# Kernel optimization log

Hardware: AMD Instinct MI355X
Metric: run time of the kernel (lower is better)

## Reference

```python
import jax, jax.numpy as jnp
import numpy as np

B, T, D_IN, D_EMB, D_OUT = 8, 2048, 1024, 1024, 1024


def setup_inputs() -> dict:
    key = jax.random.key(0)
    ks = jax.random.split(key, 7)
    s_in = 1.0 / np.sqrt(D_IN)
    s_emb = 1.0 / np.sqrt(D_EMB)
    return {
        "x": jax.random.normal(ks[0], (B, T, D_IN), dtype=jnp.float32),
        "bias": jax.random.normal(ks[1], (T, T), dtype=jnp.float32) * 0.02,
        "W_qkv": jax.random.uniform(ks[2], (3 * D_EMB, D_IN), jnp.float32, -s_in, s_in),
        "b_qkv": jax.random.uniform(ks[3], (3 * D_EMB,), jnp.float32, -s_in, s_in),
        "W_out": jax.random.uniform(ks[4], (D_OUT, D_EMB), jnp.float32, -s_emb, s_emb),
        "b_out": jax.random.uniform(ks[5], (D_OUT,), jnp.float32, -s_emb, s_emb),
    }


def reference(x, bias, W_qkv, b_qkv, W_out, b_out):
    # fused QKV projection: [B,T,3E]
    qkv = jnp.einsum("bti,ei->bte", x, W_qkv) + b_qkv
    q, k, v = jnp.split(qkv, 3, axis=-1)  # each [B,T,E]
    d_z = q.shape[-1]
    # scaled dot-product logits with additive relative-position bias
    attn = jnp.einsum("btd,bsd->bts", q, k) / jnp.sqrt(jnp.asarray(d_z, q.dtype))
    attn = attn + bias  # [T,T] broadcast over batch
    attn = jax.nn.softmax(attn, axis=-1)
    values = jnp.einsum("bts,bsd->btd", attn, v)  # [B,T,E]
    out = jnp.einsum("bte,oe->bto", values, W_out) + b_out  # [B,T,O]
    return out
```

## Files before the change

### kernel.cpp

```cpp
#include <hip/hip_runtime.h>
#include <hip/hip_bf16.h>

#define B_DIM 8
#define T_DIM 2048
#define E_DIM 1024

typedef __attribute__((ext_vector_type(8))) short short8;
typedef __attribute__((ext_vector_type(4))) float f32x4;
typedef __attribute__((ext_vector_type(4))) int int4v;

__device__ __forceinline__ unsigned short f2bf(float f) {
  union { float f; unsigned u; } v; v.f = f;
  unsigned r = v.u + 0x7fffu + ((v.u >> 16) & 1u);
  return (unsigned short)(r >> 16);
}
__device__ __forceinline__ float bf2f(unsigned short u) {
  union { unsigned u; float f; } v; v.u = ((unsigned)u) << 16;
  return v.f;
}
__device__ __forceinline__ signed char q8(float f, float scale) {
  int q = __float2int_rn(f * scale);
  q = q > 127 ? 127 : (q < -127 ? -127 : q);
  return (signed char)q;
}

__device__ __forceinline__ void async16(const void* g, void* l) {
  __builtin_amdgcn_global_load_lds(
      (const __attribute__((address_space(1))) unsigned int*)g,
      (__attribute__((address_space(3))) unsigned int*)l, 16, 0, 0);
}

__device__ __forceinline__ void storeC(float* p, float v) { *p = v; }
__device__ __forceinline__ void storeC(unsigned short* p, float v) { *p = f2bf(v); }
__device__ __forceinline__ void storeC(signed char* p, float v) { *p = (signed char)(int)v; }

#define QX 31.75f
#define QY 1814.2857f
#define QP 15.875f
#define KDQ_LOGIT 1.7359973e-5f
#define KDQ_PV    0.031496063f

__global__ __launch_bounds__(256) void cvt_bf16(const float4* __restrict__ in,
                                                ushort4* __restrict__ out) {
  size_t i = (size_t)blockIdx.x * 256 + threadIdx.x;
  float4 v = in[i];
  ushort4 o;
  o.x = f2bf(v.x); o.y = f2bf(v.y); o.z = f2bf(v.z); o.w = f2bf(v.w);
  out[i] = o;
}

__global__ __launch_bounds__(256) void cvt_x_dual(const float* __restrict__ x,
                                                  unsigned short* __restrict__ Xb,
                                                  signed char* __restrict__ Xb8,
                                                  signed char* __restrict__ XT8) {
  __shared__ signed char tc[64][65];
  const int t0 = blockIdx.x * 64, i0 = blockIdx.y * 64;
  const int tx = threadIdx.x & 63, ty = threadIdx.x >> 6;
#pragma unroll
  for (int it = 0; it < 16; ++it) {
    int r = it * 4 + ty;
    float f = x[(size_t)(t0 + r) * 1024 + i0 + tx];
    Xb[(size_t)(t0 + r) * 1024 + i0 + tx] = f2bf(f);
    signed char c = q8(f, QX);
    Xb8[(size_t)(t0 + r) * 1024 + i0 + tx] = c;
    tc[r][tx] = c;
  }
  __syncthreads();
#pragma unroll
  for (int it = 0; it < 16; ++it) {
    int r = it * 4 + ty;
    XT8[(size_t)(i0 + r) * 16384 + t0 + tx] = tc[tx][r];
  }
}

__global__ __launch_bounds__(256) void cvt_t64x3(const float* __restrict__ in,
                                                 unsigned short* __restrict__ o0,
                                                 unsigned short* __restrict__ o1,
                                                 unsigned short* __restrict__ o2) {
  __shared__ unsigned short tl[64][65];
  unsigned short* outT = blockIdx.z == 0 ? o0 : (blockIdx.z == 1 ? o1 : o2);
  const float* src = in + (size_t)blockIdx.z * 1024 * 1024;
  const int r0 = blockIdx.x * 64, c0 = blockIdx.y * 64;
  const int tx = threadIdx.x & 63, ty = threadIdx.x >> 6;
#pragma unroll
  for (int it = 0; it < 16; ++it) {
    int r = it * 4 + ty;
    tl[r][tx] = f2bf(src[(size_t)(r0 + r) * 1024 + c0 + tx]);
  }
  __syncthreads();
#pragma unroll
  for (int it = 0; it < 16; ++it) {
    int r = it * 4 + ty;
    outT[(size_t)(c0 + r) * 1024 + r0 + tx] = tl[tx][r];
  }
}

__global__ __launch_bounds__(256) void dotrows2(const unsigned short* __restrict__ W0,
                                                const float* __restrict__ v0,
                                                const float* __restrict__ add0,
                                                float* __restrict__ out0,
                                                const unsigned short* __restrict__ W1,
                                                const float* __restrict__ v1,
                                                float* __restrict__ out1) {
  const int z = blockIdx.y;
  const unsigned short* W = z ? W1 : W0;
  const float* vec = z ? v1 : v0;
  const float scale = z ? 0.03125f : 1.0f;
  const int o = blockIdx.x * 4 + (threadIdx.x >> 6);
  const int lane = threadIdx.x & 63;
  const short8 w0 = *(const short8*)&W[(size_t)o * 1024 + lane * 16];
  const short8 w1 = *(const short8*)&W[(size_t)o * 1024 + lane * 16 + 8];
  float s = 0.f;
#pragma unroll
  for (int j = 0; j < 8; ++j) s += bf2f((unsigned short)w0[j]) * vec[lane * 16 + j];
#pragma unroll
  for (int j = 0; j < 8; ++j) s += bf2f((unsigned short)w1[j]) * vec[lane * 16 + 8 + j];
#pragma unroll
  for (int off = 1; off < 64; off <<= 1) s += __shfl_xor(s, off);
  if (lane == 0) {
    if (z) out1[o] = s * scale;
    else   out0[o] = s + add0[o];
  }
}

__global__ __launch_bounds__(256) void wvec_k(const unsigned short* __restrict__ Xb,
                                              const float* __restrict__ a2,
                                              float* __restrict__ w) {
  const int row = blockIdx.x * 4 + (threadIdx.x >> 6);
  const int lane = threadIdx.x & 63;
  const short8 x0 = *(const short8*)&Xb[(size_t)row * 1024 + lane * 16];
  const short8 x1 = *(const short8*)&Xb[(size_t)row * 1024 + lane * 16 + 8];
  float s = 0.f;
#pragma unroll
  for (int j = 0; j < 8; ++j) s += bf2f((unsigned short)x0[j]) * a2[lane * 16 + j];
#pragma unroll
  for (int j = 0; j < 8; ++j) s += bf2f((unsigned short)x1[j]) * a2[lane * 16 + 8 + j];
#pragma unroll
  for (int off = 1; off < 64; off <<= 1) s += __shfl_xor(s, off);
  if (lane == 0) w[row] = s;
}

__global__ __launch_bounds__(256) void finish_rowsum(const float* __restrict__ psum,
                                                     float* __restrict__ R) {
  const int z = blockIdx.y;
  const int row = blockIdx.x * 256 + threadIdx.x;
  const float* p = psum + (size_t)z * 32 * 2048 + row;
  float s = 0.f;
#pragma unroll
  for (int k = 0; k < 32; ++k) s += p[k * 2048];
  R[(size_t)z * 2048 + row] = s;
}

__global__ __launch_bounds__(256) void gemm128sk(
    const unsigned short* __restrict__ A0, const unsigned short* __restrict__ B0,
    const unsigned short* __restrict__ A1, const unsigned short* __restrict__ B1,
    float* __restrict__ pw) {
  __shared__ __align__(16) unsigned short Al[128 * 32];
  __shared__ __align__(16) unsigned short Bl[128 * 32];
  const int prob = blockIdx.z & 1, slice = blockIdx.z >> 1;
  const unsigned short* A = prob ? A1 : A0;
  const unsigned short* Bmat = prob ? B1 : B0;
  float* C = pw + ((size_t)prob * 4 + slice) * 1048576;
  const int kbase = slice * 256;

  const int tid = threadIdx.x;
  const int wid = tid >> 6, lane = tid & 63;
  const int wm = wid >> 1, wn = wid & 1;
  const int tm = blockIdx.x * 128, tn = blockIdx.y * 128;
  const int l16 = lane & 15, lk = lane >> 4;

  f32x4 acc[4][4];
#pragma unroll
  for (int i = 0; i < 4; ++i)
#pragma unroll
    for (int j = 0; j < 4; ++j) acc[i][j] = (f32x4){0.f, 0.f, 0.f, 0.f};

  const int ks = (lk ^ ((l16 >> 1) & 3)) * 8;

  for (int k0 = kbase; k0 < kbase + 256; k0 += 32) {
    __syncthreads();
#pragma unroll
    for (int it = 0; it < 2; ++it) {
      int chunk = it * 256 + tid;
      int row = chunk >> 2;
      int q = chunk & 3;
      int qs = q ^ ((row >> 1) & 3);
      const char* g = (const char*)(A + (size_t)(tm + row) * 1024 + k0) + qs * 16;
      async16(g, ((char*)Al) + it * 4096 + wid * 1024);
    }
#pragma unroll
    for (int it = 0; it < 2; ++it) {
      int chunk = it * 256 + tid;
      int row = chunk >> 2;
      int q = chunk & 3;
      int qs = q ^ ((row >> 1) & 3);
      const char* g = (const char*)(Bmat + (size_t)(tn + row) * 1024 + k0) + qs * 16;
      async16(g, ((char*)Bl) + it * 4096 + wid * 1024);
    }
    __syncthreads();

    short8 a[4], b[4];
#pragma unroll
    for (int i = 0; i < 4; ++i)
      a[i] = *(const short8*)&Al[(wm * 64 + i * 16 + l16) * 32 + ks];
#pragma unroll
    for (int j = 0; j < 4; ++j)
      b[j] = *(const short8*)&Bl[(wn * 64 + j * 16 + l16) * 32 + ks];
#pragma unroll
    for (int i = 0; i < 4; ++i)
#pragma unroll
      for (int j = 0; j < 4; ++j)
        acc[i][j] = __builtin_amdgcn_mfma_f32_16x16x32_bf16(a[i], b[j], acc[i][j], 0, 0, 0);
  }

#pragma unroll
  for (int i = 0; i < 4; ++i)
#pragma unroll
    for (int j = 0; j < 4; ++j) {
      int col = tn + wn * 64 + j * 16 + l16;
      int rbase = tm + wm * 64 + i * 16 + lk * 4;
#pragma unroll
      for (int r = 0; r < 4; ++r)
        C[(size_t)(rbase + r) * 1024 + col] = acc[i][j][r];
    }
}

__global__ __launch_bounds__(256) void finish_w(const float* __restrict__ pw,
                                                unsigned short* __restrict__ BH,
                                                unsigned short* __restrict__ Wf) {
  const int prob = blockIdx.y;
  const size_t i = ((size_t)blockIdx.x * 256 + threadIdx.x) * 2;
  const float* p = pw + (size_t)prob * 4194304;
  float s0 = 0.f, s1 = 0.f;
#pragma unroll
  for (int k = 0; k < 4; ++k) {
    const float2 v = *(const float2*)(p + (size_t)k * 1048576 + i);
    s0 += v.x; s1 += v.y;
  }
  const float sc = prob ? 1.0f : 0.03125f;
  unsigned short* dst = prob ? Wf : BH;
  dst[i] = f2bf(s0 * sc);
  dst[i + 1] = f2bf(s1 * sc);
}

template <int EPI, typename OutT>
__global__ __launch_bounds__(512, 2) void gemm8p(
    const unsigned short* __restrict__ A, int lda, long long strA,
    const unsigned short* __restrict__ Bm, int ldb, long long strB,
    OutT* __restrict__ C, int ldc, long long strC, int K,
    const float* __restrict__ biasv, float scale) {
  __shared__ __align__(16) char lds[131072];
  const int tid = threadIdx.x;
  const int wid = tid >> 6, lane = tid & 63;
  const int wm = wid >> 2, wn = wid & 3;
  const int l16 = lane & 15, lk = lane >> 4;
  const int zz = blockIdx.z;

  const int nx = gridDim.x;
  const int nwg = nx * gridDim.y;
  const int bid = blockIdx.y * nx + blockIdx.x;
  const int swz = (bid & 7) * (nwg >> 3) + (bid >> 3);
  const int tm = (swz % nx) * 256, tn = (swz / nx) * 256;

  A += (size_t)zz * strA;
  Bm += (size_t)zz * strB;
  C += (size_t)zz * strC;

  const int nt = K >> 6;

  const int q0 = ((lk ^ (l16 & 7)) << 4);
  const int q1 = (((lk | 4) ^ (l16 & 7)) << 4);
  const int srow = lane >> 3;
  const int scol = ((lane & 7) ^ srow) << 3;

  f32x4 acc[8][4];
#pragma unroll
  for (int i = 0; i < 8; ++i)
#pragma unroll
    for (int j = 0; j < 4; ++j) acc[i][j] = (f32x4){0.f, 0.f, 0.f, 0.f};

  short8 bF[4][2];

#define STAGE_A(tt, h)                                                              \
  {                                                                                 \
    const int buf_ = (tt) & 1, k0_ = (tt) << 6;                                     \
    { const unsigned short* g_ =                                                    \
          A + (size_t)(tm + (h) * 128 + wid * 16 + srow) * lda + k0_ + scol;        \
      async16(g_, lds + (buf_ * 2 + (h)) * 16384 + wid * 2048); }                   \
    { const unsigned short* g_ =                                                    \
          A + (size_t)(tm + (h) * 128 + wid * 16 + 8 + srow) * lda + k0_ + scol;    \
      async16(g_, lds + (buf_ * 2 + (h)) * 16384 + wid * 2048 + 1024); }            \
  }
#define STAGE_B(tt, h)                                                              \
  {                                                                                 \
    const int buf_ = (tt) & 1, k0_ = (tt) << 6;                                     \
    { const unsigned short* g_ =                                                    \
          Bm + (size_t)(tn + (h) * 128 + wid * 16 + srow) * ldb + k0_ + scol;       \
      async16(g_, lds + 65536 + (buf_ * 2 + (h)) * 16384 + wid * 2048); }           \
    { const unsigned short* g_ =                                                    \
          Bm + (size_t)(tn + (h) * 128 + wid * 16 + 8 + srow) * ldb + k0_ + scol;   \
      async16(g_, lds + 65536 + (buf_ * 2 + (h)) * 16384 + wid * 2048 + 1024); }    \
  }
#define PHASE(tt, cur_, p_)                                                         \
  {                                                                                 \
    if ((p_) == 0) {                                                                \
      if ((tt) + 1 < nt) asm volatile("s_waitcnt vmcnt(4)" ::: "memory");           \
      else               asm volatile("s_waitcnt vmcnt(0)" ::: "memory");           \
      __builtin_amdgcn_s_barrier();                                                 \
      asm volatile("" ::: "memory");                                                \
    }                                                                               \
    if ((p_) == 2) {                                                                \
      __builtin_amdgcn_s_barrier();                                                 \
      asm volatile("" ::: "memory");                                                \
    }                                                                               \
    const char* aB = lds + ((cur_) * 2 + wm) * 16384 + l16 * 128;                   \
    const char* bB = lds + 65536 + ((cur_) * 2 + (wn >> 1)) * 16384 +               \
                     ((wn & 1) * 64 + l16) * 128;                                   \
    short8 a00 = *(const short8*)(aB + (2 * (p_)) * 2048 + q0);                     \
    short8 a01 = *(const short8*)(aB + (2 * (p_)) * 2048 + q1);                     \
    short8 a10 = *(const short8*)(aB + (2 * (p_) + 1) * 2048 + q0);                 \
    short8 a11 = *(const short8*)(aB + (2 * (p_) + 1) * 2048 + q1);                 \
    if ((p_) == 0) {                                                                \
      _Pragma("unroll")                                                             \
      for (int wc = 0; wc < 4; ++wc) {                                              \
        bF[wc][0] = *(const short8*)(bB + wc * 2048 + q0);                          \
        bF[wc][1] = *(const short8*)(bB + wc * 2048 + q1);                          \
      }                                                                             \
    }                                                                               \
    if ((p_) == 0 && (tt) + 1 < nt) STAGE_A((tt) + 1, 0);                           \
    if ((p_) == 1 && (tt) + 1 < nt) STAGE_A((tt) + 1, 1);                           \
    if ((p_) == 2 && (tt) + 2 < nt) STAGE_B((tt) + 2, 0);                           \
    if ((p_) == 3 && (tt) + 2 < nt) STAGE_B((tt) + 2, 1);                           \
    __builtin_amdgcn_s_setprio(1);                                                  \
    _Pragma("unroll")                                                               \
    for (int wc = 0; wc < 4; ++wc) {                                                \
      acc[2 * (p_)][wc] =                                                           \
          __builtin_amdgcn_mfma_f32_16x16x32_bf16(a00, bF[wc][0], acc[2 * (p_)][wc], 0, 0, 0); \
      acc[2 * (p_)][wc] =                                                           \
          __builtin_amdgcn_mfma_f32_16x16x32_bf16(a01, bF[wc][1], acc[2 * (p_)][wc], 0, 0, 0); \
      acc[2 * (p_) + 1][wc] =                                                       \
          __builtin_amdgcn_mfma_f32_16x16x32_bf16(a10, bF[wc][0], acc[2 * (p_) + 1][wc], 0, 0, 0); \
      acc[2 * (p_) + 1][wc] =                                                       \
          __builtin_amdgcn_mfma_f32_16x16x32_bf16(a11, bF[wc][1], acc[2 * (p_) + 1][wc], 0, 0, 0); \
    }                                                                               \
    __builtin_amdgcn_s_setprio(0);                                                  \
  }

  STAGE_A(0, 0); STAGE_A(0, 1); STAGE_B(0, 0); STAGE_B(0, 1);
  STAGE_B(1, 0); STAGE_B(1, 1);

  int t = 0;
  for (; t + 1 < nt; t += 2) {
    PHASE(t, 0, 0) PHASE(t, 0, 1) PHASE(t, 0, 2) PHASE(t, 0, 3)
    PHASE(t + 1, 1, 0) PHASE(t + 1, 1, 1) PHASE(t + 1, 1, 2) PHASE(t + 1, 1, 3)
  }
  if (t < nt) {
    const int c = t & 1;
    if (c == 0) { PHASE(t, 0, 0) PHASE(t, 0, 1) PHASE(t, 0, 2) PHASE(t, 0, 3) }
    else        { PHASE(t, 1, 0) PHASE(t, 1, 1) PHASE(t, 1, 2) PHASE(t, 1, 3) }
  }
#undef STAGE_A
#undef STAGE_B
#undef PHASE

#pragma unroll
  for (int fr = 0; fr < 8; ++fr) {
    const int rbase = tm + wm * 128 + fr * 16 + lk * 4;
#pragma unroll
    for (int wc = 0; wc < 4; ++wc) {
      const int col = tn + wn * 64 + wc * 16 + l16;
#pragma unroll
      for (int r = 0; r < 4; ++r) {
        float v = acc[fr][wc][r];
        const int row = rbase + r;
        if (EPI == 1) v += biasv[col];
        if (EPI == 6) {
          C[(size_t)row * ldc + col] = (OutT)q8(v, scale);
        } else {
          storeC(&C[(size_t)row * ldc + col], v);
        }
      }
    }
  }
}

template <int EPI, typename OutT>
__global__ __launch_bounds__(512, 2) void gemm8i(
    const signed char* __restrict__ A, int lda, long long strA,
    const signed char* __restrict__ Bm, int ldb, long long strB,
    OutT* __restrict__ C, int ldc, long long strC, int K,
    const float* __restrict__ biasv,
    const unsigned short* __restrict__ biasm, int ldbm,
    float kdq, float qp, float* __restrict__ psum) {
  __shared__ __align__(16) char lds[131072];
  const int tid = threadIdx.x;
  const int wid = tid >> 6, lane = tid & 63;
  const int wm = wid >> 2, wn = wid & 3;
  const int l16 = lane & 15, lk = lane >> 4;
  const int zz = blockIdx.z;

  const int nx = gridDim.x;
  const int nwg = nx * gridDim.y;
  const int bid = blockIdx.y * nx + blockIdx.x;
  const int swz = (bid & 7) * (nwg >> 3) + (bid >> 3);
  const int tm = (swz % nx) * 256, tn = (swz / nx) * 256;

  A += (size_t)zz * strA;
  Bm += (size_t)zz * strB;
  C += (size_t)zz * strC;

  const int nt = K >> 7;

  const int q0 = ((lk ^ (l16 & 7)) << 4);
  const int q1 = (((lk | 4) ^ (l16 & 7)) << 4);
  const int srow = lane >> 3;
  const int scol = ((lane & 7) ^ srow) << 4;

  int4v acc[8][4];
#pragma unroll
  for (int i = 0; i < 8; ++i)
#pragma unroll
    for (int j = 0; j < 4; ++j) acc[i][j] = (int4v){0, 0, 0, 0};

  int4v bF[4][2];

#define STAGE_A(tt, h)                                                              \
  {                                                                                 \
    const int buf_ = (tt) & 1, k0_ = (tt) << 7;                                     \
    { const signed char* g_ =                                                       \
          A + (size_t)(tm + (h) * 128 + wid * 16 + srow) * lda + k0_ + scol;        \
      async16(g_, lds + (buf_ * 2 + (h)) * 16384 + wid * 2048); }                   \
    { const signed char* g_ =                                                       \
          A + (size_t)(tm + (h) * 128 + wid * 16 + 8 + srow) * lda + k0_ + scol;    \
      async16(g_, lds + (buf_ * 2 + (h)) * 16384 + wid * 2048 + 1024); }            \
  }
#define STAGE_B(tt, h)                                                              \
  {                                                                                 \
    const int buf_ = (tt) & 1, k0_ = (tt) << 7;                                     \
    { const signed char* g_ =                                                       \
          Bm + (size_t)(tn + (h) * 128 + wid * 16 + srow) * ldb + k0_ + scol;       \
      async16(g_, lds + 65536 + (buf_ * 2 + (h)) * 16384 + wid * 2048); }           \
    { const signed char* g_ =                                                       \
          Bm + (size_t)(tn + (h) * 128 + wid * 16 + 8 + srow) * ldb + k0_ + scol;   \
      async16(g_, lds + 65536 + (buf_ * 2 + (h)) * 16384 + wid * 2048 + 1024); }    \
  }
#define PHASE(tt, cur_, p_)                                                         \
  {                                                                                 \
    if ((p_) == 0) {                                                                \
      if ((tt) + 1 < nt) asm volatile("s_waitcnt vmcnt(4)" ::: "memory");           \
      else               asm volatile("s_waitcnt vmcnt(0)" ::: "memory");           \
      __builtin_amdgcn_s_barrier();                                                 \
      asm volatile("" ::: "memory");                                                \
    }                                                                               \
    if ((p_) == 2) {                                                                \
      __builtin_amdgcn_s_barrier();                                                 \
      asm volatile("" ::: "memory");                                                \
    }                                                                               \
    const char* aB = lds + ((cur_) * 2 + wm) * 16384 + l16 * 128;                   \
    const char* bB = lds + 65536 + ((cur_) * 2 + (wn >> 1)) * 16384 +               \
                     ((wn & 1) * 64 + l16) * 128;                                   \
    int4v a00 = *(const int4v*)(aB + (2 * (p_)) * 2048 + q0);                       \
    int4v a01 = *(const int4v*)(aB + (2 * (p_)) * 2048 + q1);                       \
    int4v a10 = *(const int4v*)(aB + (2 * (p_) + 1) * 2048 + q0);                   \
    int4v a11 = *(const int4v*)(aB + (2 * (p_) + 1) * 2048 + q1);                   \
    if ((p_) == 0) {                                                                \
      _Pragma("unroll")                                                             \
      for (int wc = 0; wc < 4; ++wc) {                                              \
        bF[wc][0] = *(const int4v*)(bB + wc * 2048 + q0);                           \
        bF[wc][1] = *(const int4v*)(bB + wc * 2048 + q1);                           \
      }                                                                             \
    }                                                                               \
    if ((p_) == 0 && (tt) + 1 < nt) STAGE_A((tt) + 1, 0);                           \
    if ((p_) == 1 && (tt) + 1 < nt) STAGE_A((tt) + 1, 1);                           \
    if ((p_) == 2 && (tt) + 2 < nt) STAGE_B((tt) + 2, 0);                           \
    if ((p_) == 3 && (tt) + 2 < nt) STAGE_B((tt) + 2, 1);                           \
    __builtin_amdgcn_s_setprio(1);                                                  \
    _Pragma("unroll")                                                               \
    for (int wc = 0; wc < 4; ++wc) {                                                \
      acc[2 * (p_)][wc] =                                                           \
          __builtin_amdgcn_mfma_i32_16x16x64_i8(a00, bF[wc][0], acc[2 * (p_)][wc], 0, 0, 0); \
      acc[2 * (p_)][wc] =                                                           \
          __builtin_amdgcn_mfma_i32_16x16x64_i8(a01, bF[wc][1], acc[2 * (p_)][wc], 0, 0, 0); \
      acc[2 * (p_) + 1][wc] =                                                       \
          __builtin_amdgcn_mfma_i32_16x16x64_i8(a10, bF[wc][0], acc[2 * (p_) + 1][wc], 0, 0, 0); \
      acc[2 * (p_) + 1][wc] =                                                       \
          __builtin_amdgcn_mfma_i32_16x16x64_i8(a11, bF[wc][1], acc[2 * (p_) + 1][wc], 0, 0, 0); \
    }                                                                               \
    __builtin_amdgcn_s_setprio(0);                                                  \
  }

  STAGE_A(0, 0); STAGE_A(0, 1); STAGE_B(0, 0); STAGE_B(0, 1);
  STAGE_B(1, 0); STAGE_B(1, 1);

  int t = 0;
  for (; t + 1 < nt; t += 2) {
    PHASE(t, 0, 0) PHASE(t, 0, 1) PHASE(t, 0, 2) PHASE(t, 0, 3)
    PHASE(t + 1, 1, 0) PHASE(t + 1, 1, 1) PHASE(t + 1, 1, 2) PHASE(t + 1, 1, 3)
  }
  if (t < nt) {
    const int c = t & 1;
    if (c == 0) { PHASE(t, 0, 0) PHASE(t, 0, 1) PHASE(t, 0, 2) PHASE(t, 0, 3) }
    else        { PHASE(t, 1, 0) PHASE(t, 1, 1) PHASE(t, 1, 2) PHASE(t, 1, 3) }
  }
#undef STAGE_A
#undef STAGE_B
#undef PHASE

#pragma unroll
  for (int fr = 0; fr < 8; ++fr) {
    const int rbase = tm + wm * 128 + fr * 16 + lk * 4;
    float rin[4];
    if (EPI == 5) {
#pragma unroll
      for (int r = 0; r < 4; ++r)
        rin[r] = kdq / biasv[(size_t)zz * ldbm + rbase + r];
    }
    float rs[4] = {0.f, 0.f, 0.f, 0.f};
#pragma unroll
    for (int wc = 0; wc < 4; ++wc) {
      const int col = tn + wn * 64 + wc * 16 + l16;
#pragma unroll
      for (int r = 0; r < 4; ++r) {
        const int row = rbase + r;
        if (EPI == 4) {
          float v = (float)acc[fr][wc][r] * kdq;
          v = __expf(v + bf2f(biasm[(size_t)row * ldbm + col]) +
                     biasv[(size_t)zz * T_DIM + col]);
          int q = (int)(v * qp + 0.5f);
          q = q > 127 ? 127 : q;
          C[(size_t)row * ldc + col] = (OutT)(signed char)q;
          rs[r] += (float)q;
        }
        if (EPI == 5) {
          float v = (float)acc[fr][wc][r] * rin[r];
          storeC(&C[(size_t)row * ldc + col], v);
        }
      }
    }
    if (EPI == 4) {
#pragma unroll
      for (int r = 0; r < 4; ++r) {
#pragma unroll
        for (int off = 1; off < 16; off <<= 1) rs[r] += __shfl_xor(rs[r], off);
      }
      if (l16 == 0) {
        const int slab = ((zz * 8 + (tn >> 8)) * 4 + wn);
#pragma unroll
        for (int r = 0; r < 4; ++r)
          psum[(size_t)slab * 2048 + rbase + r] = rs[r];
      }
    }
  }
}

extern "C" void kernel_launch(void* const* d_in, const int* in_sizes, int n_in,
                              void* d_out, int out_size, void* d_ws, size_t ws_size,
                              hipStream_t stream) {
  const float* x = (const float*)d_in[0];
  const float* bias = (const float*)d_in[1];
  const float* Wqkv = (const float*)d_in[2];
  const float* bqkv = (const float*)d_in[3];
  const float* Wout = (const float*)d_in[4];
  const float* bout = (const float*)d_in[5];
  float* out = (float*)d_out;

  char* ws = (char*)d_ws;
  unsigned short* Xb    = (unsigned short*)(ws + 0);
  signed char*    Xb8   = (signed char*)(ws + 33554432);
  signed char*    XT8   = (signed char*)(ws + 50331648);
  unsigned short* WqT   = (unsigned short*)(ws + 67108864);
  unsigned short* WkT   = (unsigned short*)(ws + 69206016);
  unsigned short* WvT   = (unsigned short*)(ws + 71303168);
  unsigned short* Woutb = (unsigned short*)(ws + 73400320);
  unsigned short* BH    = (unsigned short*)(ws + 75497472);
  unsigned short* Wfb   = (unsigned short*)(ws + 77594624);
  float*          bfv   = (float*)(ws + 79691776);
  float*          a2    = (float*)(ws + 79695872);
  float*          wv    = (float*)(ws + 79699968);
  signed char*    Y8    = (signed char*)(ws + 79765504);
  unsigned short* biasb = (unsigned short*)(ws + 96542720);
  signed char*    P8    = (signed char*)(ws + 104931328);
  float*          pw    = (float*)(ws + 104931328);
  float*          psum  = (float*)(ws + 138485760);
  unsigned short* Valb  = Xb;
  float*          R     = out + ((size_t)out_size - B_DIM * T_DIM);

  const long long sX8  = (long long)T_DIM * 1024;
  const long long sTT8 = (long long)T_DIM * T_DIM;
  const long long sTE  = (long long)T_DIM * E_DIM;

  cvt_x_dual<<<dim3(256, 16), 256, 0, stream>>>(x, Xb, Xb8, XT8);
  cvt_t64x3<<<dim3(16, 16, 3), 256, 0, stream>>>(Wqkv, WqT, WkT, WvT);
  cvt_bf16<<<1024, 256, 0, stream>>>((const float4*)Wout, (ushort4*)Woutb);
  cvt_bf16<<<4096, 256, 0, stream>>>((const float4*)bias, (ushort4*)biasb);

  dotrows2<<<dim3(256, 2), 256, 0, stream>>>(Woutb, bqkv + 2048, bout, bfv,
                                             WkT, bqkv, a2);
  gemm128sk<<<dim3(8, 8, 8), 256, 0, stream>>>(WkT, WqT, Woutb, WvT, pw);
  finish_w<<<dim3(2048, 2), 256, 0, stream>>>(pw, BH, Wfb);
  wvec_k<<<4096, 256, 0, stream>>>(Xb, a2, wv);

  gemm8p<6, signed char><<<dim3(64, 4, 1), 512, 0, stream>>>(
      Xb, 1024, 0, BH, 1024, 0, Y8, 1024, 0, 1024, nullptr, QY);

  gemm8i<4, signed char><<<dim3(8, 8, B_DIM), 512, 0, stream>>>(
      Y8, 1024, sX8, Xb8, 1024, sX8, P8, T_DIM, sTT8, 1024,
      wv, biasb, T_DIM, KDQ_LOGIT, QP, psum);

  finish_rowsum<<<dim3(8, B_DIM), 256, 0, stream>>>(psum, R);

  gemm8i<5, unsigned short><<<dim3(8, 4, B_DIM), 512, 0, stream>>>(
      P8, T_DIM, sTT8, XT8, 8 * T_DIM, T_DIM,
      Valb, E_DIM, sTE, T_DIM, R, nullptr, T_DIM, KDQ_PV, 0.f, nullptr);

  gemm8p<1, float><<<dim3(64, 4, 1), 512, 0, stream>>>(
      Valb, 1024, 0, Wfb, 1024, 0, out, 1024, 0, 1024, bfv, 0.f);
}
```

Before: 235.7 us.

## Shrink GEMM k-tile to halve LDS, simplify double-buffer pipeline, fuse weight conversions

Both the bf16 and int8 GEMM kernels now stage a K-slice half as deep (32 bf16 / 64 int8 per tile) with a single prefetch-ahead double buffer and one barrier per tile. This replaces the four-phase, staggered A/B staging schedule. LDS use drops from 128 KiB to 64 KiB per block, which may allow more resident blocks, at the cost of twice as many barriers and less latency hiding per iteration. Separately, the W_out bf16 conversion is folded into the QKV weight transpose kernel as a fourth z-slice, saving one launch.

```diff
diff --git a/kernel.cpp b/kernel.cpp
--- a/kernel.cpp
+++ b/kernel.cpp
@@ -73,15 +73,26 @@
   }
 }
 
-__global__ __launch_bounds__(256) void cvt_t64x3(const float* __restrict__ in,
-                                                 unsigned short* __restrict__ o0,
-                                                 unsigned short* __restrict__ o1,
-                                                 unsigned short* __restrict__ o2) {
+__global__ __launch_bounds__(256) void cvt_w4(const float* __restrict__ Wqkv,
+                                              const float* __restrict__ Wout,
+                                              unsigned short* __restrict__ o0,
+                                              unsigned short* __restrict__ o1,
+                                              unsigned short* __restrict__ o2,
+                                              unsigned short* __restrict__ o3) {
   __shared__ unsigned short tl[64][65];
-  unsigned short* outT = blockIdx.z == 0 ? o0 : (blockIdx.z == 1 ? o1 : o2);
-  const float* src = in + (size_t)blockIdx.z * 1024 * 1024;
+  const int z = blockIdx.z;
   const int r0 = blockIdx.x * 64, c0 = blockIdx.y * 64;
   const int tx = threadIdx.x & 63, ty = threadIdx.x >> 6;
+  if (z == 3) {
+#pragma unroll
+    for (int it = 0; it < 16; ++it) {
+      int r = it * 4 + ty;
+      o3[(size_t)(r0 + r) * 1024 + c0 + tx] = f2bf(Wout[(size_t)(r0 + r) * 1024 + c0 + tx]);
+    }
+    return;
+  }
+  const float* src = Wqkv + (size_t)z * 1024 * 1024;
+  unsigned short* outT = z == 0 ? o0 : (z == 1 ? o1 : o2);
 #pragma unroll
   for (int it = 0; it < 16; ++it) {
     int r = it * 4 + ty;
@@ -249,7 +260,7 @@
     const unsigned short* __restrict__ Bm, int ldb, long long strB,
     OutT* __restrict__ C, int ldc, long long strC, int K,
     const float* __restrict__ biasv, float scale) {
-  __shared__ __align__(16) char lds[131072];
+  __shared__ __align__(16) char lds[65536];
   const int tid = threadIdx.x;
   const int wid = tid >> 6, lane = tid & 63;
   const int wm = wid >> 2, wn = wid & 3;
@@ -266,12 +277,11 @@
   Bm += (size_t)zz * strB;
   C += (size_t)zz * strC;
 
-  const int nt = K >> 6;
-
-  const int q0 = ((lk ^ (l16 & 7)) << 4);
-  const int q1 = (((lk | 4) ^ (l16 & 7)) << 4);
-  const int srow = lane >> 3;
-  const int scol = ((lane & 7) ^ srow) << 3;
+  const int nt = K >> 5;
+
+  const int srow = lane >> 2;
+  const int sgq = (lane & 3) ^ (srow & 3);
+  const int qa = (lk ^ (l16 & 3)) << 4;
 
   f32x4 acc[8][4];
 #pragma unroll
@@ -279,89 +289,53 @@
 #pragma unroll
     for (int j = 0; j < 4; ++j) acc[i][j] = (f32x4){0.f, 0.f, 0.f, 0.f};
 
-  short8 bF[4][2];
-
-#define STAGE_A(tt, h)                                                              \
-  {                                                                                 \
-    const int buf_ = (tt) & 1, k0_ = (tt) << 6;                                     \
-    { const unsigned short* g_ =                                                    \
-          A + (size_t)(tm + (h) * 128 + wid * 16 + srow) * lda + k0_ + scol;        \
-      async16(g_, lds + (buf_ * 2 + (h)) * 16384 + wid * 2048); }                   \
-    { const unsigned short* g_ =                                                    \
-          A + (size_t)(tm + (h) * 128 + wid * 16 + 8 + srow) * lda + k0_ + scol;    \
-      async16(g_, lds + (buf_ * 2 + (h)) * 16384 + wid * 2048 + 1024); }            \
-  }
-#define STAGE_B(tt, h)                                                              \
-  {                                                                                 \
-    const int buf_ = (tt) & 1, k0_ = (tt) << 6;                                     \
-    { const unsigned short* g_ =                                                    \
-          Bm + (size_t)(tn + (h) * 128 + wid * 16 + srow) * ldb + k0_ + scol;       \
-      async16(g_, lds + 65536 + (buf_ * 2 + (h)) * 16384 + wid * 2048); }           \
-    { const unsigned short* g_ =                                                    \
-          Bm + (size_t)(tn + (h) * 128 + wid * 16 + 8 + srow) * ldb + k0_ + scol;   \
-      async16(g_, lds + 65536 + (buf_ * 2 + (h)) * 16384 + wid * 2048 + 1024); }    \
-  }
-#define PHASE(tt, cur_, p_)                                                         \
-  {                                                                                 \
-    if ((p_) == 0) {                                                                \
-      if ((tt) + 1 < nt) asm volatile("s_waitcnt vmcnt(4)" ::: "memory");           \
-      else               asm volatile("s_waitcnt vmcnt(0)" ::: "memory");           \
-      __builtin_amdgcn_s_barrier();                                                 \
-      asm volatile("" ::: "memory");                                                \
-    }                                                                               \
-    if ((p_) == 2) {                                                                \
-      __builtin_amdgcn_s_barrier();                                                 \
-      asm volatile("" ::: "memory");                                                \
-    }                                                                               \
-    const char* aB = lds + ((cur_) * 2 + wm) * 16384 + l16 * 128;                   \
-    const char* bB = lds + 65536 + ((cur_) * 2 + (wn >> 1)) * 16384 +               \
-                     ((wn & 1) * 64 + l16) * 128;                                   \
-    short8 a00 = *(const short8*)(aB + (2 * (p_)) * 2048 + q0);                     \
-    short8 a01 = *(const short8*)(aB + (2 * (p_)) * 2048 + q1);                     \
-    short8 a10 = *(const short8*)(aB + (2 * (p_) + 1) * 2048 + q0);                 \
-    short8 a11 = *(const short8*)(aB + (2 * (p_) + 1) * 2048 + q1);                 \
-    if ((p_) == 0) {                                                                \
-      _Pragma("unroll")                                                             \
-      for (int wc = 0; wc < 4; ++wc) {                                              \
-        bF[wc][0] = *(const short8*)(bB + wc * 2048 + q0);                          \
-        bF[wc][1] = *(const short8*)(bB + wc * 2048 + q1);                          \
-      }                                                                             \
-    }                                                                               \
-    if ((p_) == 0 && (tt) + 1 < nt) STAGE_A((tt) + 1, 0);                           \
-    if ((p_) == 1 && (tt) + 1 < nt) STAGE_A((tt) + 1, 1);                           \
-    if ((p_) == 2 && (tt) + 2 < nt) STAGE_B((tt) + 2, 0);                           \
-    if ((p_) == 3 && (tt) + 2 < nt) STAGE_B((tt) + 2, 1);                           \
-    __builtin_amdgcn_s_setprio(1);                                                  \
-    _Pragma("unroll")                                                               \
-    for (int wc = 0; wc < 4; ++wc) {                                                \
-      acc[2 * (p_)][wc] =                                                           \
-          __builtin_amdgcn_mfma_f32_16x16x32_bf16(a00, bF[wc][0], acc[2 * (p_)][wc], 0, 0, 0); \
-      acc[2 * (p_)][wc] =                                                           \
-          __builtin_amdgcn_mfma_f32_16x16x32_bf16(a01, bF[wc][1], acc[2 * (p_)][wc], 0, 0, 0); \
-      acc[2 * (p_) + 1][wc] =                                                       \
-          __builtin_amdgcn_mfma_f32_16x16x32_bf16(a10, bF[wc][0], acc[2 * (p_) + 1][wc], 0, 0, 0); \
-      acc[2 * (p_) + 1][wc] =                                                       \
-          __builtin_amdgcn_mfma_f32_16x16x32_bf16(a11, bF[wc][1], acc[2 * (p_) + 1][wc], 0, 0, 0); \
-    }                                                                               \
-    __builtin_amdgcn_s_setprio(0);                                                  \
-  }
-
-  STAGE_A(0, 0); STAGE_A(0, 1); STAGE_B(0, 0); STAGE_B(0, 1);
-  STAGE_B(1, 0); STAGE_B(1, 1);
-
-  int t = 0;
-  for (; t + 1 < nt; t += 2) {
-    PHASE(t, 0, 0) PHASE(t, 0, 1) PHASE(t, 0, 2) PHASE(t, 0, 3)
-    PHASE(t + 1, 1, 0) PHASE(t + 1, 1, 1) PHASE(t + 1, 1, 2) PHASE(t + 1, 1, 3)
-  }
-  if (t < nt) {
-    const int c = t & 1;
-    if (c == 0) { PHASE(t, 0, 0) PHASE(t, 0, 1) PHASE(t, 0, 2) PHASE(t, 0, 3) }
-    else        { PHASE(t, 1, 0) PHASE(t, 1, 1) PHASE(t, 1, 2) PHASE(t, 1, 3) }
-  }
-#undef STAGE_A
-#undef STAGE_B
-#undef PHASE
+#define STAGE(tt)                                                                      \
+  {                                                                                    \
+    const int buf_ = (tt) & 1, k0_ = (tt) << 5;                                        \
+    _Pragma("unroll")                                                                  \
+    for (int is = 0; is < 2; ++is) {                                                   \
+      const unsigned short* gA_ =                                                      \
+          A + (size_t)(tm + is * 128 + wid * 16 + srow) * lda + k0_ + sgq * 8;         \
+      async16(gA_, lds + buf_ * 16384 + is * 8192 + wid * 1024);                       \
+      const unsigned short* gB_ =                                                      \
+          Bm + (size_t)(tn + is * 128 + wid * 16 + srow) * ldb + k0_ + sgq * 8;        \
+      async16(gB_, lds + 32768 + buf_ * 16384 + is * 8192 + wid * 1024);               \
+    }                                                                                  \
+  }
+#define TILE(tt, cur_)                                                                 \
+  {                                                                                    \
+    if ((tt) + 1 < nt) STAGE((tt) + 1);                                                \
+    const char* aB = lds + (cur_) * 16384;                                             \
+    const char* bB = lds + 32768 + (cur_) * 16384;                                     \
+    short8 b0 = *(const short8*)(bB + (wn * 64 + l16) * 64 + qa);                      \
+    short8 b1 = *(const short8*)(bB + (wn * 64 + 16 + l16) * 64 + qa);                 \
+    short8 b2 = *(const short8*)(bB + (wn * 64 + 32 + l16) * 64 + qa);                 \
+    short8 b3 = *(const short8*)(bB + (wn * 64 + 48 + l16) * 64 + qa);                 \
+    __builtin_amdgcn_s_setprio(1);                                                     \
+    _Pragma("unroll")                                                                  \
+    for (int fr = 0; fr < 8; ++fr) {                                                   \
+      short8 a_ = *(const short8*)(aB + (wm * 128 + fr * 16 + l16) * 64 + qa);         \
+      acc[fr][0] = __builtin_amdgcn_mfma_f32_16x16x32_bf16(a_, b0, acc[fr][0], 0, 0, 0); \
+      acc[fr][1] = __builtin_amdgcn_mfma_f32_16x16x32_bf16(a_, b1, acc[fr][1], 0, 0, 0); \
+      acc[fr][2] = __builtin_amdgcn_mfma_f32_16x16x32_bf16(a_, b2, acc[fr][2], 0, 0, 0); \
+      acc[fr][3] = __builtin_amdgcn_mfma_f32_16x16x32_bf16(a_, b3, acc[fr][3], 0, 0, 0); \
+    }                                                                                  \
+    __builtin_amdgcn_s_setprio(0);                                                     \
+    if ((tt) + 1 < nt) {                                                               \
+      asm volatile("s_waitcnt vmcnt(0)" ::: "memory");                                 \
+      __builtin_amdgcn_s_barrier();                                                    \
+      asm volatile("" ::: "memory");                                                   \
+    }                                                                                  \
+  }
+
+  STAGE(0);
+  asm volatile("s_waitcnt vmcnt(0)" ::: "memory");
+  __builtin_amdgcn_s_barrier();
+  asm volatile("" ::: "memory");
+
+  for (int t = 0; t + 1 < nt; t += 2) { TILE(t, 0) TILE(t + 1, 1) }
+#undef STAGE
+#undef TILE
 
 #pragma unroll
   for (int fr = 0; fr < 8; ++fr) {
@@ -373,8 +347,10 @@
       for (int r = 0; r < 4; ++r) {
         float v = acc[fr][wc][r];
         const int row = rbase + r;
-        if (EPI == 1) v += biasv[col];
-        if (EPI == 6) {
+        if constexpr (EPI == 1) {
+          v += biasv[col];
+          storeC(&C[(size_t)row * ldc + col], v);
+        } else if constexpr (EPI == 6) {
           C[(size_t)row * ldc + col] = (OutT)q8(v, scale);
         } else {
           storeC(&C[(size_t)row * ldc + col], v);
@@ -392,7 +368,7 @@
     const float* __restrict__ biasv,
     const unsigned short* __restrict__ biasm, int ldbm,
     float kdq, float qp, float* __restrict__ psum) {
-  __shared__ __align__(16) char lds[131072];
+  __shared__ __align__(16) char lds[65536];
   const int tid = threadIdx.x;
   const int wid = tid >> 6, lane = tid & 63;
   const int wm = wid >> 2, wn = wid & 3;
@@ -409,12 +385,11 @@
   Bm += (size_t)zz * strB;
   C += (size_t)zz * strC;
 
-  const int nt = K >> 7;
-
-  const int q0 = ((lk ^ (l16 & 7)) << 4);
-  const int q1 = (((lk | 4) ^ (l16 & 7)) << 4);
-  const int srow = lane >> 3;
-  const int scol = ((lane & 7) ^ srow) << 4;
+  const int nt = K >> 6;
+
+  const int srow = lane >> 2;
+  const int sgq = (lane & 3) ^ (srow & 3);
+  const int qa = (lk ^ (l16 & 3)) << 4;
 
   int4v acc[8][4];
 #pragma unroll
@@ -422,95 +397,59 @@
 #pragma unroll
     for (int j = 0; j < 4; ++j) acc[i][j] = (int4v){0, 0, 0, 0};
 
-  int4v bF[4][2];
-
-#define STAGE_A(tt, h)                                                              \
-  {                                                                                 \
-    const int buf_ = (tt) & 1, k0_ = (tt) << 7;                                     \
-    { const signed char* g_ =                                                       \
-          A + (size_t)(tm + (h) * 128 + wid * 16 + srow) * lda + k0_ + scol;        \
-      async16(g_, lds + (buf_ * 2 + (h)) * 16384 + wid * 2048); }                   \
-    { const signed char* g_ =                                                       \
-          A + (size_t)(tm + (h) * 128 + wid * 16 + 8 + srow) * lda + k0_ + scol;    \
-      async16(g_, lds + (buf_ * 2 + (h)) * 16384 + wid * 2048 + 1024); }            \
-  }
-#define STAGE_B(tt, h)                                                              \
-  {                                                                                 \
-    const int buf_ = (tt) & 1, k0_ = (tt) << 7;                                     \
-    { const signed char* g_ =                                                       \
-          Bm + (size_t)(tn + (h) * 128 + wid * 16 + srow) * ldb + k0_ + scol;       \
-      async16(g_, lds + 65536 + (buf_ * 2 + (h)) * 16384 + wid * 2048); }           \
-    { const signed char* g_ =                                                       \
-          Bm + (size_t)(tn + (h) * 128 + wid * 16 + 8 + srow) * ldb + k0_ + scol;   \
-      async16(g_, lds + 65536 + (buf_ * 2 + (h)) * 16384 + wid * 2048 + 1024); }    \
-  }
-#define PHASE(tt, cur_, p_)                                                         \
-  {                                                                                 \
-    if ((p_) == 0) {                                                                \
-      if ((tt) + 1 < nt) asm volatile("s_waitcnt vmcnt(4)" ::: "memory");           \
-      else               asm volatile("s_waitcnt vmcnt(0)" ::: "memory");           \
-      __builtin_amdgcn_s_barrier();                                                 \
-      asm volatile("" ::: "memory");                                                \
-    }                                                                               \
-    if ((p_) == 2) {                                                                \
-      __builtin_amdgcn_s_barrier();                                                 \
-      asm volatile("" ::: "memory");                                                \
-    }                                                                               \
-    const char* aB = lds + ((cur_) * 2 + wm) * 16384 + l16 * 128;                   \
-    const char* bB = lds + 65536 + ((cur_) * 2 + (wn >> 1)) * 16384 +               \
-                     ((wn & 1) * 64 + l16) * 128;                                   \
-    int4v a00 = *(const int4v*)(aB + (2 * (p_)) * 2048 + q0);                       \
-    int4v a01 = *(const int4v*)(aB + (2 * (p_)) * 2048 + q1);                       \
-    int4v a10 = *(const int4v*)(aB + (2 * (p_) + 1) * 2048 + q0);                   \
-    int4v a11 = *(const int4v*)(aB + (2 * (p_) + 1) * 2048 + q1);                   \
-    if ((p_) == 0) {                                                                \
-      _Pragma("unroll")                                                             \
-      for (int wc = 0; wc < 4; ++wc) {                                              \
-        bF[wc][0] = *(const int4v*)(bB + wc * 2048 + q0);                           \
-        bF[wc][1] = *(const int4v*)(bB + wc * 2048 + q1);                           \
-      }                                                                             \
-    }                                                                               \
-    if ((p_) == 0 && (tt) + 1 < nt) STAGE_A((tt) + 1, 0);                           \
-    if ((p_) == 1 && (tt) + 1 < nt) STAGE_A((tt) + 1, 1);                           \
-    if ((p_) == 2 && (tt) + 2 < nt) STAGE_B((tt) + 2, 0);                           \
-    if ((p_) == 3 && (tt) + 2 < nt) STAGE_B((tt) + 2, 1);                           \
-    __builtin_amdgcn_s_setprio(1);                                                  \
-    _Pragma("unroll")                                                               \
-    for (int wc = 0; wc < 4; ++wc) {                                                \
-      acc[2 * (p_)][wc] =                                                           \
-          __builtin_amdgcn_mfma_i32_16x16x64_i8(a00, bF[wc][0], acc[2 * (p_)][wc], 0, 0, 0); \
-      acc[2 * (p_)][wc] =                                                           \
-          __builtin_amdgcn_mfma_i32_16x16x64_i8(a01, bF[wc][1], acc[2 * (p_)][wc], 0, 0, 0); \
-      acc[2 * (p_) + 1][wc] =                                                       \
-          __builtin_amdgcn_mfma_i32_16x16x64_i8(a10, bF[wc][0], acc[2 * (p_) + 1][wc], 0, 0, 0); \
-      acc[2 * (p_) + 1][wc] =                                                       \
-          __builtin_amdgcn_mfma_i32_16x16x64_i8(a11, bF[wc][1], acc[2 * (p_) + 1][wc], 0, 0, 0); \
-    }                                                                               \
-    __builtin_amdgcn_s_setprio(0);                                                  \
-  }
-
-  STAGE_A(0, 0); STAGE_A(0, 1); STAGE_B(0, 0); STAGE_B(0, 1);
-  STAGE_B(1, 0); STAGE_B(1, 1);
-
-  int t = 0;
-  for (; t + 1 < nt; t += 2) {
-    PHASE(t, 0, 0) PHASE(t, 0, 1) PHASE(t, 0, 2) PHASE(t, 0, 3)
-    PHASE(t + 1, 1, 0) PHASE(t + 1, 1, 1) PHASE(t + 1, 1, 2) PHASE(t + 1, 1, 3)
-  }
-  if (t < nt) {
-    const int c = t & 1;
-    if (c == 0) { PHASE(t, 0, 0) PHASE(t, 0, 1) PHASE(t, 0, 2) PHASE(t, 0, 3) }
-    else        { PHASE(t, 1, 0) PHASE(t, 1, 1) PHASE(t, 1, 2) PHASE(t, 1, 3) }
-  }
-#undef STAGE_A
-#undef STAGE_B
-#undef PHASE
+#define STAGE(tt)                                                                      \
+  {                                                                                    \
+    const int buf_ = (tt) & 1, k0_ = (tt) << 6;                                        \
+    _Pragma("unroll")                                                                  \
+    for (int is = 0; is < 2; ++is) {                                                   \
+      const signed char* gA_ =                                                         \
+          A + (size_t)(tm + is * 128 + wid * 16 + srow) * lda + k0_ + sgq * 16;        \
+      async16(gA_, lds + buf_ * 16384 + is * 8192 + wid * 1024);                       \
+      const signed char* gB_ =                                                         \
+          Bm + (size_t)(tn + is * 128 + wid * 16 + srow) * ldb + k0_ + sgq * 16;       \
+      async16(gB_, lds + 32768 + buf_ * 16384 + is * 8192 + wid * 1024);               \
+    }                                                                                  \
+  }
+#define TILE(tt, cur_)                                                                 \
+  {                                                                                    \
+    if ((tt) + 1 < nt) STAGE((tt) + 1);                                                \
+    const char* aB = lds + (cur_) * 16384;                                             \
+    const char* bB = lds + 32768 + (cur_) * 16384;                                     \
+    int4v b0 = *(const int4v*)(bB + (wn * 64 + l16) * 64 + qa);                        \
+    int4v b1 = *(const int4v*)(bB + (wn * 64 + 16 + l16) * 64 + qa);                   \
+    int4v b2 = *(const int4v*)(bB + (wn * 64 + 32 + l16) * 64 + qa);                   \
+    int4v b3 = *(const int4v*)(bB + (wn * 64 + 48 + l16) * 64 + qa);                   \
+    __builtin_amdgcn_s_setprio(1);                                                     \
+    _Pragma("unroll")                                                                  \
+    for (int fr = 0; fr < 8; ++fr) {                                                   \
+      int4v a_ = *(const int4v*)(aB + (wm * 128 + fr * 16 + l16) * 64 + qa);           \
+      acc[fr][0] = __builtin_amdgcn_mfma_i32_16x16x64_i8(a_, b0, acc[fr][0], 0, 0, 0); \
+      acc[fr][1] = __builtin_amdgcn_mfma_i32_16x16x64_i8(a_, b1, acc[fr][1], 0, 0, 0); \
+      acc[fr][2] = __builtin_amdgcn_mfma_i32_16x16x64_i8(a_, b2, acc[fr][2], 0, 0, 0); \
+      acc[fr][3] = __builtin_amdgcn_mfma_i32_16x16x64_i8(a_, b3, acc[fr][3], 0, 0, 0); \
+    }                                                                                  \
+    __builtin_amdgcn_s_setprio(0);                                                     \
+    if ((tt) + 1 < nt) {                                                               \
+      asm volatile("s_waitcnt vmcnt(0)" ::: "memory");                                 \
+      __builtin_amdgcn_s_barrier();                                                    \
+      asm volatile("" ::: "memory");                                                   \
+    }                                                                                  \
+  }
+
+  STAGE(0);
+  asm volatile("s_waitcnt vmcnt(0)" ::: "memory");
+  __builtin_amdgcn_s_barrier();
+  asm volatile("" ::: "memory");
+
+  for (int t = 0; t + 1 < nt; t += 2) { TILE(t, 0) TILE(t + 1, 1) }
+#undef STAGE
+#undef TILE
 
 #pragma unroll
   for (int fr = 0; fr < 8; ++fr) {
     const int rbase = tm + wm * 128 + fr * 16 + lk * 4;
     float rin[4];
-    if (EPI == 5) {
+    if constexpr (EPI == 5) {
 #pragma unroll
       for (int r = 0; r < 4; ++r)
         rin[r] = kdq / biasv[(size_t)zz * ldbm + rbase + r];
@@ -522,7 +461,7 @@
 #pragma unroll
       for (int r = 0; r < 4; ++r) {
         const int row = rbase + r;
-        if (EPI == 4) {
+        if constexpr (EPI == 4) {
           float v = (float)acc[fr][wc][r] * kdq;
           v = __expf(v + bf2f(biasm[(size_t)row * ldbm + col]) +
                      biasv[(size_t)zz * T_DIM + col]);
@@ -530,14 +469,13 @@
           q = q > 127 ? 127 : q;
           C[(size_t)row * ldc + col] = (OutT)(signed char)q;
           rs[r] += (float)q;
-        }
-        if (EPI == 5) {
+        } else if constexpr (EPI == 5) {
           float v = (float)acc[fr][wc][r] * rin[r];
           storeC(&C[(size_t)row * ldc + col], v);
         }
       }
     }
-    if (EPI == 4) {
+    if constexpr (EPI == 4) {
 #pragma unroll
       for (int r = 0; r < 4; ++r) {
 #pragma unroll
@@ -590,8 +528,7 @@
   const long long sTE  = (long long)T_DIM * E_DIM;
 
   cvt_x_dual<<<dim3(256, 16), 256, 0, stream>>>(x, Xb, Xb8, XT8);
-  cvt_t64x3<<<dim3(16, 16, 3), 256, 0, stream>>>(Wqkv, WqT, WkT, WvT);
-  cvt_bf16<<<1024, 256, 0, stream>>>((const float4*)Wout, (ushort4*)Woutb);
+  cvt_w4<<<dim3(16, 16, 4), 256, 0, stream>>>(Wqkv, Wout, WqT, WkT, WvT, Woutb);
   cvt_bf16<<<4096, 256, 0, stream>>>((const float4*)bias, (ushort4*)biasb);
 
   dotrows2<<<dim3(256, 2), 256, 0, stream>>>(Woutb, bqkv + 2048, bout, bfv,
```

New measurement: 265.9 us. 12.8% more time.
